# Performance work log

Hardware: AMD Instinct MI355X
Metric: run time of the kernel (lower is better)

## Reference

```python
import jax, jax.numpy as jnp
import numpy as np

N = 50000      # nodes
E = 800000     # edges
H = 128        # hidden_features
DEPTH = 5
G = 64         # graphs in batch
EPS = 1e-5


def _ln(x, g, b):
    m = jnp.mean(x, axis=-1, keepdims=True)
    v = jnp.mean((x - m) ** 2, axis=-1, keepdims=True)
    return (x - m) * jax.lax.rsqrt(v + EPS) * g + b


def _lin_init(key, fan_in, fan_out):
    s = 1.0 / np.sqrt(fan_in)
    kw, kb = jax.random.split(key)
    return (jax.random.uniform(kw, (fan_in, fan_out), jnp.float32, -s, s),
            jax.random.uniform(kb, (fan_out,), jnp.float32, -s, s))


def setup_inputs() -> dict:
    key = jax.random.key(0)
    ks = jax.random.split(key, 16)
    inp = {
        'x': jax.random.normal(ks[0], (N, 1), jnp.float32),
        'pos': jax.random.normal(ks[1], (N, 3), jnp.float32),
        'edge_index': jax.random.randint(ks[2], (2, E), 0, N, jnp.int32),
        'cell_offset': jax.random.normal(ks[3], (E, 3), jnp.float32),
        'unit_cell': jax.random.normal(ks[4], (3, 3), jnp.float32),
        'batch_ids': jnp.sort(jax.random.randint(ks[5], (N,), 0, G, jnp.int32)),
    }
    inp['emb_w'], inp['emb_b'] = _lin_init(ks[6], 1, H)
    # stacked per-layer params for lax.scan
    def stack(fn):
        outs = [fn(jax.random.fold_in(ks[7], i)) for i in range(DEPTH)]
        return tuple(jnp.stack(t) for t in zip(*outs))
    def layer_params(k):
        k1, k2, k3, k4 = jax.random.split(k, 4)
        mw1, mb1 = _lin_init(k1, 2 * H + 1, H)
        mw2, mb2 = _lin_init(k2, H, H)
        uw1, ub1 = _lin_init(k3, 2 * H, H)
        uw2, ub2 = _lin_init(k4, H, H)
        ones = jnp.ones((H,), jnp.float32); zeros = jnp.zeros((H,), jnp.float32)
        return (mw1, mb1, ones, zeros, mw2, mb2, ones, zeros,
                uw1, ub1, ones, zeros, uw2, ub2, ones, zeros)
    (inp['msg_w1'], inp['msg_b1'], inp['msg_g1'], inp['msg_be1'],
     inp['msg_w2'], inp['msg_b2'], inp['msg_g2'], inp['msg_be2'],
     inp['upd_w1'], inp['upd_b1'], inp['upd_g1'], inp['upd_be1'],
     inp['upd_w2'], inp['upd_b2'], inp['upd_g2'], inp['upd_be2']) = stack(layer_params)
    inp['pred_w1'], inp['pred_b1'] = _lin_init(ks[8], H, H)
    inp['pred_w2'], inp['pred_b2'] = _lin_init(ks[9], H, 1)
    return inp


def reference(x, pos, edge_index, cell_offset, unit_cell, batch_ids,
              emb_w, emb_b,
              msg_w1, msg_b1, msg_g1, msg_be1, msg_w2, msg_b2, msg_g2, msg_be2,
              upd_w1, upd_b1, upd_g1, upd_be1, upd_w2, upd_b2, upd_g2, upd_be2,
              pred_w1, pred_b1, pred_w2, pred_b2):
    src, dst = edge_index[0], edge_index[1]  # PyG: x_j = source, x_i = target
    h = x @ emb_w + emb_b  # [N, H]
    # PBC distances
    corrected = pos[dst] - cell_offset @ unit_cell  # [E, 3]
    dist = jnp.linalg.norm(corrected - pos[src], axis=-1, keepdims=True)  # [E, 1]

    def step(h, p):
        (mw1, mb1, mg1, mbe1, mw2, mb2, mg2, mbe2,
         uw1, ub1, ug1, ube1, uw2, ub2, ug2, ube2) = p
        msg = jnp.concatenate([h[dst], h[src], dist], axis=-1)  # [E, 2H+1]
        msg = jax.nn.relu(_ln(msg @ mw1 + mb1, mg1, mbe1))
        msg = jax.nn.relu(_ln(msg @ mw2 + mb2, mg2, mbe2))
        aggr = jax.ops.segment_sum(msg, dst, num_segments=N)  # scatter-add to targets
        u = jnp.concatenate([h, aggr], axis=-1)  # [N, 2H]
        u = jax.nn.relu(_ln(u @ uw1 + ub1, ug1, ube1))
        u = jax.nn.relu(_ln(u @ uw2 + ub2, ug2, ube2))
        return h + u, None  # residual

    params = (msg_w1, msg_b1, msg_g1, msg_be1, msg_w2, msg_b2, msg_g2, msg_be2,
              upd_w1, upd_b1, upd_g1, upd_be1, upd_w2, upd_b2, upd_g2, upd_be2)
    h, _ = jax.lax.scan(step, h, params)
    pooled = jax.ops.segment_sum(h, batch_ids, num_segments=G)  # global_add_pool
    return jax.nn.relu(pooled @ pred_w1 + pred_b1) @ pred_w2 + pred_b2  # [G, 1]
```

## Files before the change

kernel.cpp:

```cpp
#include <hip/hip_runtime.h>

#define NN 50000
#define NE 800000
#define HD 128
#define DEPTH 5
#define NG 64
#define LNEPS 1e-5f

typedef __attribute__((ext_vector_type(8))) short bf8;
typedef __attribute__((ext_vector_type(4))) float f4;

static __device__ __forceinline__ unsigned short f2bf(float x) {
    unsigned int u = __float_as_uint(x);
    unsigned int r = (u + 0x7fffu + ((u >> 16) & 1u)) >> 16;
    return (unsigned short)r;
}

__global__ void pack_weights(const float* __restrict__ msg_w1, const float* __restrict__ msg_w2,
                             const float* __restrict__ upd_w1, const float* __restrict__ upd_w2,
                             unsigned short* __restrict__ packed) {
    const int which = blockIdx.y & 3, layer = blockIdx.y >> 2;
    const int t = blockIdx.x * 256 + threadIdx.x;
    const float* src; int K; unsigned short* dst;
    unsigned short* lbase = packed + layer * 98304;
    if (which == 0)      { src = msg_w1 + layer*257*HD; K = 256; dst = lbase; }
    else if (which == 1) { src = msg_w2 + layer*HD*HD;  K = 128; dst = lbase + 32768; }
    else if (which == 2) { src = upd_w1 + layer*256*HD; K = 256; dst = lbase + 49152; }
    else                 { src = upd_w2 + layer*HD*HD;  K = 128; dst = lbase + 81920; }
    if (t >= K * HD) return;
    const int e = t & 7, l = (t >> 3) & 63, f = (t >> 9) & 7, s = t >> 12;
    const int k = s*32 + ((l >> 4) << 3) + e;
    const int n = f*16 + (l & 15);
    dst[t] = f2bf(src[k*HD + n]);
}

__global__ void embed_kernel(const float* __restrict__ x, const float* __restrict__ emb_w,
                             const float* __restrict__ emb_b,
                             float* __restrict__ h, unsigned short* __restrict__ hb) {
    const int i = blockIdx.x * 256 + threadIdx.x;
    const int n = i >> 7, j = i & 127;
    const float v = x[n] * emb_w[j] + emb_b[j];
    h[i] = v; hb[i] = f2bf(v);
}

__global__ void hist_kernel(const int* __restrict__ ei, int* __restrict__ cnt) {
    const int e = blockIdx.x * 256 + threadIdx.x;
    atomicAdd(&cnt[ei[NE + e]], 1);
}

__global__ __launch_bounds__(1024) void scan_kernel(const int* __restrict__ cnt,
                                                    int* __restrict__ cur) {
    __shared__ int part[1024];
    const int t = threadIdx.x;
    const int per = 49;
    const int base = t * per;
    int s = 0;
    for (int i = 0; i < per; ++i) { const int idx = base + i; if (idx < NN) s += cnt[idx]; }
    part[t] = s; __syncthreads();
    for (int st = 1; st < 1024; st <<= 1) {
        const int v = (t >= st) ? part[t - st] : 0;
        __syncthreads();
        part[t] += v;
        __syncthreads();
    }
    int run = (t == 0) ? 0 : part[t - 1];
    for (int i = 0; i < per; ++i) {
        const int idx = base + i;
        if (idx < NN) { cur[idx] = run; run += cnt[idx]; }
    }
}

__global__ void scatter_kernel(const int* __restrict__ ei, int* __restrict__ cur,
                               int* __restrict__ sidx, int* __restrict__ ssrc,
                               int* __restrict__ sdst) {
    const int e = blockIdx.x * 256 + threadIdx.x;
    const int d = ei[NE + e];
    const int p = atomicAdd(&cur[d], 1);
    sidx[p] = e; ssrc[p] = ei[e]; sdst[p] = d;
}

__global__ void dist_kernel(const float* __restrict__ pos, const int* __restrict__ sidx,
                            const int* __restrict__ ssrc, const int* __restrict__ sdst,
                            const float* __restrict__ cell, const float* __restrict__ U,
                            float* __restrict__ dist) {
    const int p = blockIdx.x * 256 + threadIdx.x;
    const int e = sidx[p];
    const int s = ssrc[p], d = sdst[p];
    const float c0 = cell[e*3], c1 = cell[e*3+1], c2 = cell[e*3+2];
    const float ox = c0*U[0] + c1*U[3] + c2*U[6];
    const float oy = c0*U[1] + c1*U[4] + c2*U[7];
    const float oz = c0*U[2] + c1*U[5] + c2*U[8];
    const float dx = pos[d*3]   - ox - pos[s*3];
    const float dy = pos[d*3+1] - oy - pos[s*3+1];
    const float dz = pos[d*3+2] - oz - pos[s*3+2];
    dist[p] = sqrtf(dx*dx + dy*dy + dz*dz);
}

__global__ __launch_bounds__(256, 2) void edge_kernel(
    const unsigned short* __restrict__ hb, const float* __restrict__ dist,
    const int* __restrict__ ssrc, const int* __restrict__ sdst,
    const unsigned short* __restrict__ pw,
    const float* __restrict__ w1last, const float* __restrict__ b1,
    const float* __restrict__ g1, const float* __restrict__ be1,
    const float* __restrict__ b2, const float* __restrict__ g2,
    const float* __restrict__ be2, float* __restrict__ aggr)
{
    __shared__ unsigned short lds[128 * 128];
    __shared__ int dstl[128];
    char* ldsb = (char*)lds;
    const int tid = threadIdx.x, blk = blockIdx.x;
    const int l = tid & 63, wv = tid >> 6;
    const int li = l & 15, gq = l >> 4;

    if (tid < 128) dstl[tid] = sdst[blk*128 + tid];

    const int rowA = wv*32 + li, rowB = rowA + 16;
    const int eA = blk*128 + rowA, eB = blk*128 + rowB;
    const unsigned short* pDA = hb + sdst[eA]*HD + gq*8;
    const unsigned short* pSA = hb + ssrc[eA]*HD + gq*8;
    const unsigned short* pDB = hb + sdst[eB]*HD + gq*8;
    const unsigned short* pSB = hb + ssrc[eB]*HD + gq*8;

    f4 acc[2][8];
    #pragma unroll
    for (int m = 0; m < 2; ++m)
        #pragma unroll
        for (int f = 0; f < 8; ++f) { f4 z = {0.f,0.f,0.f,0.f}; acc[m][f] = z; }

    #pragma unroll
    for (int s = 0; s < 8; ++s) {
        bf8 breg[8];
        #pragma unroll
        for (int f = 0; f < 8; ++f) breg[f] = *(const bf8*)(pw + s*4096 + f*512 + l*8);
        const bf8 aA = (s < 4) ? *(const bf8*)(pDA + s*32) : *(const bf8*)(pSA + (s-4)*32);
        const bf8 aB = (s < 4) ? *(const bf8*)(pDB + s*32) : *(const bf8*)(pSB + (s-4)*32);
        #pragma unroll
        for (int f = 0; f < 8; ++f) {
            acc[0][f] = __builtin_amdgcn_mfma_f32_16x16x32_bf16(aA, breg[f], acc[0][f], 0, 0, 0);
            acc[1][f] = __builtin_amdgcn_mfma_f32_16x16x32_bf16(aB, breg[f], acc[1][f], 0, 0, 0);
        }
    }

    float bb[8], wl[8];
    #pragma unroll
    for (int f = 0; f < 8; ++f) { const int n = f*16 + li; bb[f] = b1[n]; wl[f] = w1last[n]; }
    #pragma unroll
    for (int m = 0; m < 2; ++m) {
        float dsv[4];
        #pragma unroll
        for (int r = 0; r < 4; ++r) dsv[r] = dist[blk*128 + wv*32 + m*16 + gq*4 + r];
        float ps[4] = {0,0,0,0}, pq[4] = {0,0,0,0};
        #pragma unroll
        for (int f = 0; f < 8; ++f)
            #pragma unroll
            for (int r = 0; r < 4; ++r) {
                const float v = acc[m][f][r] + bb[f] + dsv[r]*wl[f];
                ps[r] += v; pq[r] += v*v;
            }
        #pragma unroll
        for (int mm = 1; mm < 16; mm <<= 1)
            #pragma unroll
            for (int r = 0; r < 4; ++r) {
                ps[r] += __shfl_xor(ps[r], mm);
                pq[r] += __shfl_xor(pq[r], mm);
            }
        #pragma unroll
        for (int r = 0; r < 4; ++r) {
            const float mean = ps[r] * (1.f/HD);
            const float rstd = rsqrtf(pq[r]*(1.f/HD) - mean*mean + LNEPS);
            const int row = wv*32 + m*16 + gq*4 + r;
            const int rsw = (row & 7) << 4;
            #pragma unroll
            for (int f = 0; f < 8; ++f) {
                const int n = f*16 + li;
                float v = (acc[m][f][r] + bb[f] + dsv[r]*wl[f] - mean)*rstd*g1[n] + be1[n];
                *(unsigned short*)(ldsb + ((row*256 + n*2) ^ rsw)) = f2bf(fmaxf(v, 0.f));
            }
        }
    }

    const unsigned short* pw2 = pw + 32768;
    f4 acc2[2][8];
    #pragma unroll
    for (int m = 0; m < 2; ++m)
        #pragma unroll
        for (int f = 0; f < 8; ++f) { f4 z = {0.f,0.f,0.f,0.f}; acc2[m][f] = z; }
    #pragma unroll
    for (int s = 0; s < 4; ++s) {
        bf8 breg[8];
        #pragma unroll
        for (int f = 0; f < 8; ++f) breg[f] = *(const bf8*)(pw2 + s*4096 + f*512 + l*8);
        #pragma unroll
        for (int m = 0; m < 2; ++m) {
            const int ar = wv*32 + m*16 + li;
            const bf8 a = *(const bf8*)(ldsb + ((ar*256 + s*64 + gq*16) ^ ((ar & 7) << 4)));
            #pragma unroll
            for (int f = 0; f < 8; ++f)
                acc2[m][f] = __builtin_amdgcn_mfma_f32_16x16x32_bf16(a, breg[f], acc2[m][f], 0, 0, 0);
        }
    }

    float bb2[8], gg2[8], bee2[8];
    #pragma unroll
    for (int f = 0; f < 8; ++f) {
        const int n = f*16 + li;
        bb2[f] = b2[n]; gg2[f] = g2[n]; bee2[f] = be2[n];
    }
    #pragma unroll
    for (int m = 0; m < 2; ++m) {
        float ps[4] = {0,0,0,0}, pq[4] = {0,0,0,0};
        #pragma unroll
        for (int f = 0; f < 8; ++f)
            #pragma unroll
            for (int r = 0; r < 4; ++r) {
                const float v = acc2[m][f][r] + bb2[f];
                ps[r] += v; pq[r] += v*v;
            }
        #pragma unroll
        for (int mm = 1; mm < 16; mm <<= 1)
            #pragma unroll
            for (int r = 0; r < 4; ++r) {
                ps[r] += __shfl_xor(ps[r], mm);
                pq[r] += __shfl_xor(pq[r], mm);
            }
        #pragma unroll
        for (int r = 0; r < 4; ++r) {
            const float mean = ps[r] * (1.f/HD);
            const float rstd = rsqrtf(pq[r]*(1.f/HD) - mean*mean + LNEPS);
            const int row = wv*32 + m*16 + gq*4 + r;
            const int rsw = (row & 7) << 4;
            #pragma unroll
            for (int f = 0; f < 8; ++f) {
                const int n = f*16 + li;
                float v = (acc2[m][f][r] + bb2[f] - mean)*rstd*gg2[f] + bee2[f];
                *(unsigned short*)(ldsb + ((row*256 + n*2) ^ rsw)) = f2bf(fmaxf(v, 0.f));
            }
        }
    }
    __syncthreads();

    {
        const int j = tid & 127, hh = tid >> 7;
        const int r0 = hh * 64;
        int curd = dstl[r0];
        float a0 = 0.f;
        #pragma unroll 4
        for (int i = 0; i < 64; ++i) {
            const int row = r0 + i;
            const int d = dstl[row];
            const unsigned short u = *(const unsigned short*)(ldsb + ((row*256 + j*2) ^ ((row & 7) << 4)));
            const float v = __uint_as_float(((unsigned int)u) << 16);
            if (d != curd) { unsafeAtomicAdd(&aggr[curd*HD + j], a0); a0 = 0.f; curd = d; }
            a0 += v;
        }
        unsafeAtomicAdd(&aggr[curd*HD + j], a0);
    }
}

__global__ __launch_bounds__(256, 2) void node_kernel(
    unsigned short* __restrict__ hb, float* __restrict__ aggr,
    const unsigned short* __restrict__ pw,
    const float* __restrict__ b1, const float* __restrict__ g1, const float* __restrict__ be1,
    const float* __restrict__ b2, const float* __restrict__ g2, const float* __restrict__ be2,
    float* __restrict__ h)
{
    __shared__ unsigned short lds[128 * 128];
    char* ldsb = (char*)lds;
    const int tid = threadIdx.x, blk = blockIdx.x;
    const int l = tid & 63, wv = tid >> 6;
    const int li = l & 15, gq = l >> 4;

    const int rowA = wv*32 + li, rowB = rowA + 16;
    const int nA = blk*128 + rowA, nB = blk*128 + rowB;
    const int ncA = (nA < NN) ? nA : NN - 1;
    const int ncB = (nB < NN) ? nB : NN - 1;
    const unsigned short* pHA = hb + ncA*HD + gq*8;
    const unsigned short* pHB = hb + ncB*HD + gq*8;
    float* pAA = aggr + ncA*HD + gq*8;
    float* pAB = aggr + ncB*HD + gq*8;

    f4 acc[2][8];
    #pragma unroll
    for (int m = 0; m < 2; ++m)
        #pragma unroll
        for (int f = 0; f < 8; ++f) { f4 z = {0.f,0.f,0.f,0.f}; acc[m][f] = z; }

    #pragma unroll
    for (int s = 0; s < 8; ++s) {
        bf8 breg[8];
        #pragma unroll
        for (int f = 0; f < 8; ++f) breg[f] = *(const bf8*)(pw + s*4096 + f*512 + l*8);
        bf8 aA, aB;
        if (s < 4) {
            aA = *(const bf8*)(pHA + s*32);
            aB = *(const bf8*)(pHB + s*32);
        } else {
            const float4 a0 = *(const float4*)(pAA + (s-4)*32);
            const float4 a1 = *(const float4*)(pAA + (s-4)*32 + 4);
            const float4 b0 = *(const float4*)(pAB + (s-4)*32);
            const float4 b1v = *(const float4*)(pAB + (s-4)*32 + 4);
            union { unsigned short u[8]; bf8 v; } pk;
            pk.u[0]=f2bf(a0.x); pk.u[1]=f2bf(a0.y); pk.u[2]=f2bf(a0.z); pk.u[3]=f2bf(a0.w);
            pk.u[4]=f2bf(a1.x); pk.u[5]=f2bf(a1.y); pk.u[6]=f2bf(a1.z); pk.u[7]=f2bf(a1.w);
            aA = pk.v;
            pk.u[0]=f2bf(b0.x); pk.u[1]=f2bf(b0.y); pk.u[2]=f2bf(b0.z); pk.u[3]=f2bf(b0.w);
            pk.u[4]=f2bf(b1v.x); pk.u[5]=f2bf(b1v.y); pk.u[6]=f2bf(b1v.z); pk.u[7]=f2bf(b1v.w);
            aB = pk.v;
        }
        #pragma unroll
        for (int f = 0; f < 8; ++f) {
            acc[0][f] = __builtin_amdgcn_mfma_f32_16x16x32_bf16(aA, breg[f], acc[0][f], 0, 0, 0);
            acc[1][f] = __builtin_amdgcn_mfma_f32_16x16x32_bf16(aB, breg[f], acc[1][f], 0, 0, 0);
        }
    }

    {
        const float4 z = {0.f,0.f,0.f,0.f};
        #pragma unroll
        for (int s = 0; s < 4; ++s) {
            if (nA < NN) { *(float4*)(pAA + s*32) = z; *(float4*)(pAA + s*32 + 4) = z; }
            if (nB < NN) { *(float4*)(pAB + s*32) = z; *(float4*)(pAB + s*32 + 4) = z; }
        }
    }

    float bb[8];
    #pragma unroll
    for (int f = 0; f < 8; ++f) bb[f] = b1[f*16 + li];
    #pragma unroll
    for (int m = 0; m < 2; ++m) {
        float ps[4] = {0,0,0,0}, pq[4] = {0,0,0,0};
        #pragma unroll
        for (int f = 0; f < 8; ++f)
            #pragma unroll
            for (int r = 0; r < 4; ++r) {
                const float v = acc[m][f][r] + bb[f];
                ps[r] += v; pq[r] += v*v;
            }
        #pragma unroll
        for (int mm = 1; mm < 16; mm <<= 1)
            #pragma unroll
            for (int r = 0; r < 4; ++r) {
                ps[r] += __shfl_xor(ps[r], mm);
                pq[r] += __shfl_xor(pq[r], mm);
            }
        #pragma unroll
        for (int r = 0; r < 4; ++r) {
            const float mean = ps[r] * (1.f/HD);
            const float rstd = rsqrtf(pq[r]*(1.f/HD) - mean*mean + LNEPS);
            const int row = wv*32 + m*16 + gq*4 + r;
            const int rsw = (row & 7) << 4;
            #pragma unroll
            for (int f = 0; f < 8; ++f) {
                const int n = f*16 + li;
                float v = (acc[m][f][r] + bb[f] - mean)*rstd*g1[n] + be1[n];
                *(unsigned short*)(ldsb + ((row*256 + n*2) ^ rsw)) = f2bf(fmaxf(v, 0.f));
            }
        }
    }

    const unsigned short* pw2 = pw + 32768;
    f4 acc2[2][8];
    #pragma unroll
    for (int m = 0; m < 2; ++m)
        #pragma unroll
        for (int f = 0; f < 8; ++f) { f4 z = {0.f,0.f,0.f,0.f}; acc2[m][f] = z; }
    #pragma unroll
    for (int s = 0; s < 4; ++s) {
        bf8 breg[8];
        #pragma unroll
        for (int f = 0; f < 8; ++f) breg[f] = *(const bf8*)(pw2 + s*4096 + f*512 + l*8);
        #pragma unroll
        for (int m = 0; m < 2; ++m) {
            const int ar = wv*32 + m*16 + li;
            const bf8 a = *(const bf8*)(ldsb + ((ar*256 + s*64 + gq*16) ^ ((ar & 7) << 4)));
            #pragma unroll
            for (int f = 0; f < 8; ++f)
                acc2[m][f] = __builtin_amdgcn_mfma_f32_16x16x32_bf16(a, breg[f], acc2[m][f], 0, 0, 0);
        }
    }

    float bb2[8];
    #pragma unroll
    for (int f = 0; f < 8; ++f) bb2[f] = b2[f*16 + li];
    #pragma unroll
    for (int m = 0; m < 2; ++m) {
        float ps[4] = {0,0,0,0}, pq[4] = {0,0,0,0};
        #pragma unroll
        for (int f = 0; f < 8; ++f)
            #pragma unroll
            for (int r = 0; r < 4; ++r) {
                const float v = acc2[m][f][r] + bb2[f];
                ps[r] += v; pq[r] += v*v;
            }
        #pragma unroll
        for (int mm = 1; mm < 16; mm <<= 1)
            #pragma unroll
            for (int r = 0; r < 4; ++r) {
                ps[r] += __shfl_xor(ps[r], mm);
                pq[r] += __shfl_xor(pq[r], mm);
            }
        #pragma unroll
        for (int r = 0; r < 4; ++r) {
            const int node = blk*128 + wv*32 + m*16 + gq*4 + r;
            if (node < NN) {
                const float mean = ps[r] * (1.f/HD);
                const float rstd = rsqrtf(pq[r]*(1.f/HD) - mean*mean + LNEPS);
                #pragma unroll
                for (int f = 0; f < 8; ++f) {
                    const int n = f*16 + li;
                    float v = (acc2[m][f][r] + bb2[f] - mean)*rstd*g2[n] + be2[n];
                    v = fmaxf(v, 0.f);
                    const int idx = node*HD + n;
                    const float nh = h[idx] + v;
                    h[idx] = nh;
                    hb[idx] = f2bf(nh);
                }
            }
        }
    }
}

__global__ void pool_kernel(const float* __restrict__ h, const int* __restrict__ bids,
                            float* __restrict__ pooled) {
    const int j = threadIdx.x;
    const int n0 = blockIdx.x * 256;
    if (n0 >= NN) return;
    int cur = bids[n0];
    float acc = 0.f;
    for (int i = 0; i < 256; ++i) {
        const int n = n0 + i;
        if (n >= NN) break;
        const int b = bids[n];
        if (b != cur) { unsafeAtomicAdd(&pooled[cur*HD + j], acc); acc = 0.f; cur = b; }
        acc += h[n*HD + j];
    }
    unsafeAtomicAdd(&pooled[cur*HD + j], acc);
}

__global__ void pred_kernel(const float* __restrict__ pooled, const float* __restrict__ w1,
                            const float* __restrict__ pb1, const float* __restrict__ w2,
                            const float* __restrict__ pb2, float* __restrict__ out) {
    const int g = blockIdx.x, j = threadIdx.x;
    __shared__ float pg[128];
    __shared__ float red[128];
    pg[j] = pooled[g*HD + j];
    __syncthreads();
    float z = pb1[j];
    for (int k = 0; k < 128; ++k) z += pg[k] * w1[k*HD + j];
    red[j] = fmaxf(z, 0.f) * w2[j];
    __syncthreads();
    for (int st = 64; st > 0; st >>= 1) {
        if (j < st) red[j] += red[j + st];
        __syncthreads();
    }
    if (j == 0) out[g] = red[0] + pb2[0];
}

extern "C" void kernel_launch(void* const* d_in, const int* in_sizes, int n_in,
                              void* d_out, int out_size, void* d_ws, size_t ws_size,
                              hipStream_t stream) {
    const float* x       = (const float*)d_in[0];
    const float* pos     = (const float*)d_in[1];
    const int*   ei      = (const int*)  d_in[2];
    const float* cell    = (const float*)d_in[3];
    const float* U       = (const float*)d_in[4];
    const int*   bids    = (const int*)  d_in[5];
    const float* emb_w   = (const float*)d_in[6];
    const float* emb_b   = (const float*)d_in[7];
    const float* msg_w1  = (const float*)d_in[8];
    const float* msg_b1  = (const float*)d_in[9];
    const float* msg_g1  = (const float*)d_in[10];
    const float* msg_be1 = (const float*)d_in[11];
    const float* msg_w2  = (const float*)d_in[12];
    const float* msg_b2  = (const float*)d_in[13];
    const float* msg_g2  = (const float*)d_in[14];
    const float* msg_be2 = (const float*)d_in[15];
    const float* upd_w1  = (const float*)d_in[16];
    const float* upd_b1  = (const float*)d_in[17];
    const float* upd_g1  = (const float*)d_in[18];
    const float* upd_be1 = (const float*)d_in[19];
    const float* upd_w2  = (const float*)d_in[20];
    const float* upd_b2  = (const float*)d_in[21];
    const float* upd_g2  = (const float*)d_in[22];
    const float* upd_be2 = (const float*)d_in[23];
    const float* pred_w1 = (const float*)d_in[24];
    const float* pred_b1 = (const float*)d_in[25];
    const float* pred_w2 = (const float*)d_in[26];
    const float* pred_b2 = (const float*)d_in[27];

    char* ws = (char*)d_ws;
    float*          h      = (float*)          ws;
    unsigned short* hb     = (unsigned short*)(ws + 25600000);
    float*          aggr   = (float*)         (ws + 38400000);
    float*          dist   = (float*)         (ws + 64000000);
    float*          pooled = (float*)         (ws + 67200000);
    unsigned short* packed = (unsigned short*)(ws + 67232768);
    int*            cnt    = (int*)           (ws + 68215808);
    int*            cur    = (int*)           (ws + 68416512);
    int*            sidx   = (int*)           (ws + 68617216);
    int*            ssrc   = (int*)           (ws + 71817216);
    int*            sdst   = (int*)           (ws + 75017216);

    hipMemsetAsync(aggr, 0, (size_t)NN * HD * sizeof(float), stream);
    hipMemsetAsync(pooled, 0, (size_t)NG * HD * sizeof(float), stream);
    hipMemsetAsync(cnt, 0, (size_t)NN * sizeof(int), stream);

    dim3 pgrid(128, DEPTH * 4);
    pack_weights<<<pgrid, 256, 0, stream>>>(msg_w1, msg_w2, upd_w1, upd_w2, packed);
    embed_kernel<<<(NN * HD) / 256, 256, 0, stream>>>(x, emb_w, emb_b, h, hb);

    hist_kernel<<<NE / 256, 256, 0, stream>>>(ei, cnt);
    scan_kernel<<<1, 1024, 0, stream>>>(cnt, cur);
    scatter_kernel<<<NE / 256, 256, 0, stream>>>(ei, cur, sidx, ssrc, sdst);
    dist_kernel<<<NE / 256, 256, 0, stream>>>(pos, sidx, ssrc, sdst, cell, U, dist);

    for (int layer = 0; layer < DEPTH; ++layer) {
        const unsigned short* pl = packed + layer * 98304;
        edge_kernel<<<NE / 128, 256, 0, stream>>>(
            hb, dist, ssrc, sdst, pl,
            msg_w1 + layer*257*HD + 256*HD,
            msg_b1 + layer*HD, msg_g1 + layer*HD, msg_be1 + layer*HD,
            msg_b2 + layer*HD, msg_g2 + layer*HD, msg_be2 + layer*HD,
            aggr);
        node_kernel<<<(NN + 127) / 128, 256, 0, stream>>>(
            hb, aggr, pl + 49152,
            upd_b1 + layer*HD, upd_g1 + layer*HD, upd_be1 + layer*HD,
            upd_b2 + layer*HD, upd_g2 + layer*HD, upd_be2 + layer*HD,
            h);
    }

    pool_kernel<<<(NN + 255) / 256, 128, 0, stream>>>(h, bids, pooled);
    pred_kernel<<<NG, 128, 0, stream>>>(pooled, pred_w1, pred_b1, pred_w2, pred_b2, (float*)d_out);
}
```

Before: 1.507 ms.

## Pack LN outputs to LDS with 128-bit stores via permuted hidden layout

Replaces the software bf16 rounding with the hardware packed v_cvt_pk_bf16_f32 instruction. Permutes the column order of intermediate LDS tiles so each lane writes its eight features as one 16-byte store instead of eight 2-byte stores. The second-layer weights are packed with the matching row permutation, and the scatter-add remaps columns back. It also caches gamma/beta in registers, loads dist as float4, and drops the dst LDS staging in favor of direct global reads. The permutation must stay consistent across weight packing, the GEMM A reads and the aggregation, which adds correctness risk.

```diff
diff --git a/kernel.cpp b/kernel.cpp
--- a/kernel.cpp
+++ b/kernel.cpp
@@ -10,10 +10,13 @@
 typedef __attribute__((ext_vector_type(8))) short bf8;
 typedef __attribute__((ext_vector_type(4))) float f4;
 
-static __device__ __forceinline__ unsigned short f2bf(float x) {
-    unsigned int u = __float_as_uint(x);
-    unsigned int r = (u + 0x7fffu + ((u >> 16) & 1u)) >> 16;
-    return (unsigned short)r;
+static __device__ __forceinline__ unsigned int cvt2bf(float a, float b) {
+    unsigned int r;
+    asm("v_cvt_pk_bf16_f32 %0, %1, %2" : "=v"(r) : "v"(a), "v"(b));
+    return r;
+}
+static __device__ __forceinline__ unsigned short bf1(float x) {
+    return (unsigned short)cvt2bf(x, x);
 }
 
 __global__ void pack_weights(const float* __restrict__ msg_w1, const float* __restrict__ msg_w2,
@@ -29,9 +32,10 @@
     else                 { src = upd_w2 + layer*HD*HD;  K = 128; dst = lbase + 81920; }
     if (t >= K * HD) return;
     const int e = t & 7, l = (t >> 3) & 63, f = (t >> 9) & 7, s = t >> 12;
-    const int k = s*32 + ((l >> 4) << 3) + e;
+    const int kk = s*32 + ((l >> 4) << 3) + e;
+    const int k = (which & 1) ? ((kk & 7)*16 + (kk >> 3)) : kk;
     const int n = f*16 + (l & 15);
-    dst[t] = f2bf(src[k*HD + n]);
+    dst[t] = bf1(src[k*HD + n]);
 }
 
 __global__ void embed_kernel(const float* __restrict__ x, const float* __restrict__ emb_w,
@@ -40,7 +44,7 @@
     const int i = blockIdx.x * 256 + threadIdx.x;
     const int n = i >> 7, j = i & 127;
     const float v = x[n] * emb_w[j] + emb_b[j];
-    h[i] = v; hb[i] = f2bf(v);
+    h[i] = v; hb[i] = bf1(v);
 }
 
 __global__ void hist_kernel(const int* __restrict__ ei, int* __restrict__ cnt) {
@@ -106,13 +110,10 @@
     const float* __restrict__ be2, float* __restrict__ aggr)
 {
     __shared__ unsigned short lds[128 * 128];
-    __shared__ int dstl[128];
     char* ldsb = (char*)lds;
     const int tid = threadIdx.x, blk = blockIdx.x;
     const int l = tid & 63, wv = tid >> 6;
     const int li = l & 15, gq = l >> 4;
-
-    if (tid < 128) dstl[tid] = sdst[blk*128 + tid];
 
     const int rowA = wv*32 + li, rowB = rowA + 16;
     const int eA = blk*128 + rowA, eB = blk*128 + rowB;
@@ -141,40 +142,46 @@
         }
     }
 
-    float bb[8], wl[8];
-    #pragma unroll
-    for (int f = 0; f < 8; ++f) { const int n = f*16 + li; bb[f] = b1[n]; wl[f] = w1last[n]; }
-    #pragma unroll
-    for (int m = 0; m < 2; ++m) {
-        float dsv[4];
-        #pragma unroll
-        for (int r = 0; r < 4; ++r) dsv[r] = dist[blk*128 + wv*32 + m*16 + gq*4 + r];
-        float ps[4] = {0,0,0,0}, pq[4] = {0,0,0,0};
-        #pragma unroll
-        for (int f = 0; f < 8; ++f)
+    {
+        float bb[8], wl[8], gg[8], be[8];
+        #pragma unroll
+        for (int f = 0; f < 8; ++f) {
+            const int n = f*16 + li;
+            bb[f] = b1[n]; wl[f] = w1last[n]; gg[f] = g1[n]; be[f] = be1[n];
+        }
+        #pragma unroll
+        for (int m = 0; m < 2; ++m) {
+            const float4 d4 = *(const float4*)(dist + blk*128 + wv*32 + m*16 + gq*4);
+            const float dsv[4] = {d4.x, d4.y, d4.z, d4.w};
+            float ps[4] = {0,0,0,0}, pq[4] = {0,0,0,0};
+            #pragma unroll
+            for (int f = 0; f < 8; ++f)
+                #pragma unroll
+                for (int r = 0; r < 4; ++r) {
+                    const float v = acc[m][f][r] + bb[f] + dsv[r]*wl[f];
+                    acc[m][f][r] = v;
+                    ps[r] += v; pq[r] += v*v;
+                }
+            #pragma unroll
+            for (int mm = 1; mm < 16; mm <<= 1)
+                #pragma unroll
+                for (int r = 0; r < 4; ++r) {
+                    ps[r] += __shfl_xor(ps[r], mm);
+                    pq[r] += __shfl_xor(pq[r], mm);
+                }
             #pragma unroll
             for (int r = 0; r < 4; ++r) {
-                const float v = acc[m][f][r] + bb[f] + dsv[r]*wl[f];
-                ps[r] += v; pq[r] += v*v;
-            }
-        #pragma unroll
-        for (int mm = 1; mm < 16; mm <<= 1)
-            #pragma unroll
-            for (int r = 0; r < 4; ++r) {
-                ps[r] += __shfl_xor(ps[r], mm);
-                pq[r] += __shfl_xor(pq[r], mm);
-            }
-        #pragma unroll
-        for (int r = 0; r < 4; ++r) {
-            const float mean = ps[r] * (1.f/HD);
-            const float rstd = rsqrtf(pq[r]*(1.f/HD) - mean*mean + LNEPS);
-            const int row = wv*32 + m*16 + gq*4 + r;
-            const int rsw = (row & 7) << 4;
-            #pragma unroll
-            for (int f = 0; f < 8; ++f) {
-                const int n = f*16 + li;
-                float v = (acc[m][f][r] + bb[f] + dsv[r]*wl[f] - mean)*rstd*g1[n] + be1[n];
-                *(unsigned short*)(ldsb + ((row*256 + n*2) ^ rsw)) = f2bf(fmaxf(v, 0.f));
+                const float mean = ps[r] * (1.f/HD);
+                const float rstd = rsqrtf(pq[r]*(1.f/HD) - mean*mean + LNEPS);
+                const int row = wv*32 + m*16 + gq*4 + r;
+                float vv[8];
+                #pragma unroll
+                for (int f = 0; f < 8; ++f)
+                    vv[f] = fmaxf((acc[m][f][r] - mean)*rstd*gg[f] + be[f], 0.f);
+                uint4 u;
+                u.x = cvt2bf(vv[0], vv[1]); u.y = cvt2bf(vv[2], vv[3]);
+                u.z = cvt2bf(vv[4], vv[5]); u.w = cvt2bf(vv[6], vv[7]);
+                *(uint4*)(ldsb + ((row*256 + li*16) ^ ((row & 7) << 4))) = u;
             }
         }
     }
@@ -200,40 +207,44 @@
         }
     }
 
-    float bb2[8], gg2[8], bee2[8];
-    #pragma unroll
-    for (int f = 0; f < 8; ++f) {
-        const int n = f*16 + li;
-        bb2[f] = b2[n]; gg2[f] = g2[n]; bee2[f] = be2[n];
-    }
-    #pragma unroll
-    for (int m = 0; m < 2; ++m) {
-        float ps[4] = {0,0,0,0}, pq[4] = {0,0,0,0};
-        #pragma unroll
-        for (int f = 0; f < 8; ++f)
+    {
+        float bb2[8], gg2[8], be2v[8];
+        #pragma unroll
+        for (int f = 0; f < 8; ++f) {
+            const int n = f*16 + li;
+            bb2[f] = b2[n]; gg2[f] = g2[n]; be2v[f] = be2[n];
+        }
+        #pragma unroll
+        for (int m = 0; m < 2; ++m) {
+            float ps[4] = {0,0,0,0}, pq[4] = {0,0,0,0};
+            #pragma unroll
+            for (int f = 0; f < 8; ++f)
+                #pragma unroll
+                for (int r = 0; r < 4; ++r) {
+                    const float v = acc2[m][f][r] + bb2[f];
+                    acc2[m][f][r] = v;
+                    ps[r] += v; pq[r] += v*v;
+                }
+            #pragma unroll
+            for (int mm = 1; mm < 16; mm <<= 1)
+                #pragma unroll
+                for (int r = 0; r < 4; ++r) {
+                    ps[r] += __shfl_xor(ps[r], mm);
+                    pq[r] += __shfl_xor(pq[r], mm);
+                }
             #pragma unroll
             for (int r = 0; r < 4; ++r) {
-                const float v = acc2[m][f][r] + bb2[f];
-                ps[r] += v; pq[r] += v*v;
-            }
-        #pragma unroll
-        for (int mm = 1; mm < 16; mm <<= 1)
-            #pragma unroll
-            for (int r = 0; r < 4; ++r) {
-                ps[r] += __shfl_xor(ps[r], mm);
-                pq[r] += __shfl_xor(pq[r], mm);
-            }
-        #pragma unroll
-        for (int r = 0; r < 4; ++r) {
-            const float mean = ps[r] * (1.f/HD);
-            const float rstd = rsqrtf(pq[r]*(1.f/HD) - mean*mean + LNEPS);
-            const int row = wv*32 + m*16 + gq*4 + r;
-            const int rsw = (row & 7) << 4;
-            #pragma unroll
-            for (int f = 0; f < 8; ++f) {
-                const int n = f*16 + li;
-                float v = (acc2[m][f][r] + bb2[f] - mean)*rstd*gg2[f] + bee2[f];
-                *(unsigned short*)(ldsb + ((row*256 + n*2) ^ rsw)) = f2bf(fmaxf(v, 0.f));
+                const float mean = ps[r] * (1.f/HD);
+                const float rstd = rsqrtf(pq[r]*(1.f/HD) - mean*mean + LNEPS);
+                const int row = wv*32 + m*16 + gq*4 + r;
+                float vv[8];
+                #pragma unroll
+                for (int f = 0; f < 8; ++f)
+                    vv[f] = fmaxf((acc2[m][f][r] - mean)*rstd*gg2[f] + be2v[f], 0.f);
+                uint4 u;
+                u.x = cvt2bf(vv[0], vv[1]); u.y = cvt2bf(vv[2], vv[3]);
+                u.z = cvt2bf(vv[4], vv[5]); u.w = cvt2bf(vv[6], vv[7]);
+                *(uint4*)(ldsb + ((row*256 + li*16) ^ ((row & 7) << 4))) = u;
             }
         }
     }
@@ -242,18 +253,19 @@
     {
         const int j = tid & 127, hh = tid >> 7;
         const int r0 = hh * 64;
-        int curd = dstl[r0];
+        const int jj = (j & 7)*16 + (j >> 3);
+        int curd = sdst[blk*128 + r0];
         float a0 = 0.f;
         #pragma unroll 4
         for (int i = 0; i < 64; ++i) {
             const int row = r0 + i;
-            const int d = dstl[row];
+            const int d = sdst[blk*128 + row];
             const unsigned short u = *(const unsigned short*)(ldsb + ((row*256 + j*2) ^ ((row & 7) << 4)));
             const float v = __uint_as_float(((unsigned int)u) << 16);
-            if (d != curd) { unsafeAtomicAdd(&aggr[curd*HD + j], a0); a0 = 0.f; curd = d; }
+            if (d != curd) { unsafeAtomicAdd(&aggr[curd*HD + jj], a0); a0 = 0.f; curd = d; }
             a0 += v;
         }
-        unsafeAtomicAdd(&aggr[curd*HD + j], a0);
+        unsafeAtomicAdd(&aggr[curd*HD + jj], a0);
     }
 }
 
@@ -297,14 +309,14 @@
         } else {
             const float4 a0 = *(const float4*)(pAA + (s-4)*32);
             const float4 a1 = *(const float4*)(pAA + (s-4)*32 + 4);
-            const float4 b0 = *(const float4*)(pAB + (s-4)*32);
-            const float4 b1v = *(const float4*)(pAB + (s-4)*32 + 4);
-            union { unsigned short u[8]; bf8 v; } pk;
-            pk.u[0]=f2bf(a0.x); pk.u[1]=f2bf(a0.y); pk.u[2]=f2bf(a0.z); pk.u[3]=f2bf(a0.w);
-            pk.u[4]=f2bf(a1.x); pk.u[5]=f2bf(a1.y); pk.u[6]=f2bf(a1.z); pk.u[7]=f2bf(a1.w);
+            const float4 c0 = *(const float4*)(pAB + (s-4)*32);
+            const float4 c1 = *(const float4*)(pAB + (s-4)*32 + 4);
+            union { unsigned int u[4]; bf8 v; } pk;
+            pk.u[0] = cvt2bf(a0.x, a0.y); pk.u[1] = cvt2bf(a0.z, a0.w);
+            pk.u[2] = cvt2bf(a1.x, a1.y); pk.u[3] = cvt2bf(a1.z, a1.w);
             aA = pk.v;
-            pk.u[0]=f2bf(b0.x); pk.u[1]=f2bf(b0.y); pk.u[2]=f2bf(b0.z); pk.u[3]=f2bf(b0.w);
-            pk.u[4]=f2bf(b1v.x); pk.u[5]=f2bf(b1v.y); pk.u[6]=f2bf(b1v.z); pk.u[7]=f2bf(b1v.w);
+            pk.u[0] = cvt2bf(c0.x, c0.y); pk.u[1] = cvt2bf(c0.z, c0.w);
+            pk.u[2] = cvt2bf(c1.x, c1.y); pk.u[3] = cvt2bf(c1.z, c1.w);
             aB = pk.v;
         }
         #pragma unroll
@@ -323,37 +335,44 @@
         }
     }
 
-    float bb[8];
-    #pragma unroll
-    for (int f = 0; f < 8; ++f) bb[f] = b1[f*16 + li];
-    #pragma unroll
-    for (int m = 0; m < 2; ++m) {
-        float ps[4] = {0,0,0,0}, pq[4] = {0,0,0,0};
-        #pragma unroll
-        for (int f = 0; f < 8; ++f)
+    {
+        float bb[8], gg[8], be[8];
+        #pragma unroll
+        for (int f = 0; f < 8; ++f) {
+            const int n = f*16 + li;
+            bb[f] = b1[n]; gg[f] = g1[n]; be[f] = be1[n];
+        }
+        #pragma unroll
+        for (int m = 0; m < 2; ++m) {
+            float ps[4] = {0,0,0,0}, pq[4] = {0,0,0,0};
+            #pragma unroll
+            for (int f = 0; f < 8; ++f)
+                #pragma unroll
+                for (int r = 0; r < 4; ++r) {
+                    const float v = acc[m][f][r] + bb[f];
+                    acc[m][f][r] = v;
+                    ps[r] += v; pq[r] += v*v;
+                }
+            #pragma unroll
+            for (int mm = 1; mm < 16; mm <<= 1)
+                #pragma unroll
+                for (int r = 0; r < 4; ++r) {
+                    ps[r] += __shfl_xor(ps[r], mm);
+                    pq[r] += __shfl_xor(pq[r], mm);
+                }
             #pragma unroll
             for (int r = 0; r < 4; ++r) {
-                const float v = acc[m][f][r] + bb[f];
-                ps[r] += v; pq[r] += v*v;
-            }
-        #pragma unroll
-        for (int mm = 1; mm < 16; mm <<= 1)
-            #pragma unroll
-            for (int r = 0; r < 4; ++r) {
-                ps[r] += __shfl_xor(ps[r], mm);
-                pq[r] += __shfl_xor(pq[r], mm);
-            }
-        #pragma unroll
-        for (int r = 0; r < 4; ++r) {
-            const float mean = ps[r] * (1.f/HD);
-            const float rstd = rsqrtf(pq[r]*(1.f/HD) - mean*mean + LNEPS);
-            const int row = wv*32 + m*16 + gq*4 + r;
-            const int rsw = (row & 7) << 4;
-            #pragma unroll
-            for (int f = 0; f < 8; ++f) {
-                const int n = f*16 + li;
-                float v = (acc[m][f][r] + bb[f] - mean)*rstd*g1[n] + be1[n];
-                *(unsigned short*)(ldsb + ((row*256 + n*2) ^ rsw)) = f2bf(fmaxf(v, 0.f));
+                const float mean = ps[r] * (1.f/HD);
+                const float rstd = rsqrtf(pq[r]*(1.f/HD) - mean*mean + LNEPS);
+                const int row = wv*32 + m*16 + gq*4 + r;
+                float vv[8];
+                #pragma unroll
+                for (int f = 0; f < 8; ++f)
+                    vv[f] = fmaxf((acc[m][f][r] - mean)*rstd*gg[f] + be[f], 0.f);
+                uint4 u;
+                u.x = cvt2bf(vv[0], vv[1]); u.y = cvt2bf(vv[2], vv[3]);
+                u.z = cvt2bf(vv[4], vv[5]); u.w = cvt2bf(vv[6], vv[7]);
+                *(uint4*)(ldsb + ((row*256 + li*16) ^ ((row & 7) << 4))) = u;
             }
         }
     }
@@ -379,41 +398,47 @@
         }
     }
 
-    float bb2[8];
-    #pragma unroll
-    for (int f = 0; f < 8; ++f) bb2[f] = b2[f*16 + li];
-    #pragma unroll
-    for (int m = 0; m < 2; ++m) {
-        float ps[4] = {0,0,0,0}, pq[4] = {0,0,0,0};
-        #pragma unroll
-        for (int f = 0; f < 8; ++f)
+    {
+        float bb2[8], gg2[8], be2v[8];
+        #pragma unroll
+        for (int f = 0; f < 8; ++f) {
+            const int n = f*16 + li;
+            bb2[f] = b2[n]; gg2[f] = g2[n]; be2v[f] = be2[n];
+        }
+        #pragma unroll
+        for (int m = 0; m < 2; ++m) {
+            float ps[4] = {0,0,0,0}, pq[4] = {0,0,0,0};
+            #pragma unroll
+            for (int f = 0; f < 8; ++f)
+                #pragma unroll
+                for (int r = 0; r < 4; ++r) {
+                    const float v = acc2[m][f][r] + bb2[f];
+                    acc2[m][f][r] = v;
+                    ps[r] += v; pq[r] += v*v;
+                }
+            #pragma unroll
+            for (int mm = 1; mm < 16; mm <<= 1)
+                #pragma unroll
+                for (int r = 0; r < 4; ++r) {
+                    ps[r] += __shfl_xor(ps[r], mm);
+                    pq[r] += __shfl_xor(pq[r], mm);
+                }
             #pragma unroll
             for (int r = 0; r < 4; ++r) {
-                const float v = acc2[m][f][r] + bb2[f];
-                ps[r] += v; pq[r] += v*v;
-            }
-        #pragma unroll
-        for (int mm = 1; mm < 16; mm <<= 1)
-            #pragma unroll
-            for (int r = 0; r < 4; ++r) {
-                ps[r] += __shfl_xor(ps[r], mm);
-                pq[r] += __shfl_xor(pq[r], mm);
-            }
-        #pragma unroll
-        for (int r = 0; r < 4; ++r) {
-            const int node = blk*128 + wv*32 + m*16 + gq*4 + r;
-            if (node < NN) {
-                const float mean = ps[r] * (1.f/HD);
-                const float rstd = rsqrtf(pq[r]*(1.f/HD) - mean*mean + LNEPS);
-                #pragma unroll
-                for (int f = 0; f < 8; ++f) {
-                    const int n = f*16 + li;
-                    float v = (acc2[m][f][r] + bb2[f] - mean)*rstd*g2[n] + be2[n];
-                    v = fmaxf(v, 0.f);
-                    const int idx = node*HD + n;
-                    const float nh = h[idx] + v;
-                    h[idx] = nh;
-                    hb[idx] = f2bf(nh);
+                const int node = blk*128 + wv*32 + m*16 + gq*4 + r;
+                if (node < NN) {
+                    const float mean = ps[r] * (1.f/HD);
+                    const float rstd = rsqrtf(pq[r]*(1.f/HD) - mean*mean + LNEPS);
+                    #pragma unroll
+                    for (int f = 0; f < 8; ++f) {
+                        const int n = f*16 + li;
+                        float v = (acc2[m][f][r] - mean)*rstd*gg2[f] + be2v[f];
+                        v = fmaxf(v, 0.f);
+                        const int idx = node*HD + n;
+                        const float nh = h[idx] + v;
+                        h[idx] = nh;
+                        hb[idx] = bf1(nh);
+                    }
                 }
             }
         }
```

After: 1.875 ms. 24.4% more time.
